# Optimization experiments

Measured on AMD Instinct MI355X. Metric: run time of the kernel, lower is better.

Reference implementation:

```python
import jax, jax.numpy as jnp
import numpy as np

F_DIM = 128; K_RBF = 64; NBLOCKS = 3; NUM_SCC = 1; IBEGIN = 4
N_RES_INT = 2; N_RES_AT = 2; N_RES_OUT = 1
NUM_OUTPUTS = 2001; NOUTS = NUM_OUTPUTS + 4  # +4 charge-equilibration channels when num_scc>0
N_ATOMS = 10000; DEG = 32; N_EDGES = N_ATOMS * DEG; NMOL = 64
CUTOFF = 10.0
LOG2 = 0.6931471805599453


def ssp(x):
    # shifted softplus
    return jax.nn.softplus(x) - LOG2


def _residual(x, W1, b1, W2, b2):
    y = ssp(x) @ W1 + b1
    return x + ssp(y) @ W2 + b2


def _forward(R, M, QaAlpha, QaBeta,
             em_W0, em_b0, em_W1, em_b1, em_W2, em_b2,
             iWrbf, iWi, ibi, iWj, ibj, irW1, irb1, irW2, irb2, iWout, ibout, iu,
             arW1, arb1, arW2, arb2, orW1, orb1, orW2, orb2, oW,
             Z, idx_i, idx_j, mol_idx):
    N = R.shape[0]
    dt = R.dtype
    # --- interatomic distances via neighbor gather ---
    Dvec = R[idx_i] - R[idx_j]                                # [E,3]
    Dij = jnp.sqrt(jax.nn.relu(jnp.sum(Dvec * Dvec, -1)))     # [E]
    # --- PhysNet-style exp-Gaussian RBF expansion with smooth cutoff ---
    mu = jnp.linspace(np.exp(-CUTOFF), 1.0, K_RBF).astype(dt)
    gamma = jnp.asarray((K_RBF / (2.0 * (1.0 - np.exp(-CUTOFF)))) ** 2, dt)
    t = Dij / CUTOFF
    cut = jnp.where(Dij < CUTOFF, 1.0 - 6.0 * t**5 + 15.0 * t**4 - 10.0 * t**3, 0.0)
    rbf = cut[:, None] * jnp.exp(-gamma * (jnp.exp(-Dij)[:, None] - mu) ** 2)  # [E,K]

    seg_mol = lambda v: jax.ops.segment_sum(v, mol_idx, num_segments=NMOL)
    Zf = Z.astype(dt)[:, None]
    QaA, QaB = QaAlpha, QaBeta
    QAlpha_mol = seg_mol(QaA)
    QBeta_mol = seg_mol(QaB)
    outputs = None
    nhloss = jnp.asarray(0.0, dt)
    for j in range(NUM_SCC + 1):
        # elemental-modes embedding: f = [Z, M, QaAlpha, QaBeta] -> F
        f = jnp.concatenate([Zf, M[:, None], QaA[:, None], QaB[:, None]], 1)  # [N,4]
        h = ssp(f @ em_W0 + em_b0)
        h = ssp(h @ em_W1 + em_b1)
        x = h @ em_W2 + em_b2                                 # [N,F]
        outputs = jnp.zeros((N, NOUTS), dt)
        nhloss = jnp.asarray(0.0, dt)
        lastout2 = None
        for i in range(NBLOCKS):
            # --- interaction (message passing: gather -> multiply -> segment_sum) ---
            xa = ssp(x)
            g = rbf @ iWrbf[i]                                # [E,F]
            xi = ssp(xa @ iWi[i] + ibi[i])                    # [N,F]
            xj = ssp(xa @ iWj[i] + ibj[i])                    # [N,F]
            m = xi + jax.ops.segment_sum(g * xj[idx_j], idx_i, num_segments=N)
            for r in range(N_RES_INT):
                m = _residual(m, irW1[i, r], irb1[i, r], irW2[i, r], irb2[i, r])
            m = ssp(m)
            x = iu[i] * x + m @ iWout[i] + ibout[i]           # gated update
            for r in range(N_RES_AT):
                x = _residual(x, arW1[i, r], arb1[i, r], arW2[i, r], arb2[i, r])
            # --- output block ---
            xo = x
            for r in range(N_RES_OUT):
                xo = _residual(xo, orW1[i, r], orb1[i, r], orW2[i, r], orb2[i, r])
            out = ssp(xo) @ oW[i]                             # [N,NOUTS]
            outputs = outputs + out
            if j == NUM_SCC:
                out2 = out[IBEGIN:] ** 2                      # row slice, as in source
                if i > 0:
                    nhloss = nhloss + jnp.mean(out2 / (out2 + lastout2 + 1e-7))
                lastout2 = out2
        # --- NSE charge equilibration (per-molecule segment sums) ---
        QaA_n, faA = outputs[:, 0], outputs[:, 1]
        QaB_n, faB = outputs[:, 2], outputs[:, 3]
        QaA = QaA_n + faA * ((QAlpha_mol - seg_mol(QaA_n)) / seg_mol(faA))[mol_idx]
        QaB = QaB_n + faB * ((QBeta_mol - seg_mol(QaB_n)) / seg_mol(faB))[mol_idx]
    outputs = outputs[:, IBEGIN:]
    outputs = jnp.concatenate([outputs[:, :1], jax.nn.relu(outputs[:, 1:])], 1)
    return outputs, Dij, nhloss


def setup_inputs() -> dict:
    key = jax.random.key(0)
    ks = iter(jax.random.split(key, 64))
    nrm = lambda shp, scale: jax.random.normal(next(ks), shp, jnp.float32) * scale
    F, K, B = F_DIM, K_RBF, NBLOCKS
    s = F ** -0.5
    inp = {}
    inp["R"] = jax.random.uniform(next(ks), (N_ATOMS, 3), jnp.float32, 0.0, 12.0)
    inp["M"] = jax.random.uniform(next(ks), (N_ATOMS,), jnp.float32, 1.0, 32.0)
    inp["QaAlpha"] = nrm((N_ATOMS,), 0.1)
    inp["QaBeta"] = nrm((N_ATOMS,), 0.1)
    # elemental-modes MLP 4 -> F -> F -> F
    inp["em_W0"] = nrm((4, F), 0.5); inp["em_b0"] = nrm((F,), 0.01)
    inp["em_W1"] = nrm((F, F), s);   inp["em_b1"] = nrm((F,), 0.01)
    inp["em_W2"] = nrm((F, F), s);   inp["em_b2"] = nrm((F,), 0.01)
    # interaction blocks (stacked over NBLOCKS)
    inp["iWrbf"] = nrm((B, K, F), K ** -0.5)
    inp["iWi"] = nrm((B, F, F), s); inp["ibi"] = nrm((B, F), 0.01)
    inp["iWj"] = nrm((B, F, F), s); inp["ibj"] = nrm((B, F), 0.01)
    inp["irW1"] = nrm((B, N_RES_INT, F, F), s); inp["irb1"] = nrm((B, N_RES_INT, F), 0.01)
    inp["irW2"] = nrm((B, N_RES_INT, F, F), s); inp["irb2"] = nrm((B, N_RES_INT, F), 0.01)
    inp["iWout"] = nrm((B, F, F), s); inp["ibout"] = nrm((B, F), 0.01)
    inp["iu"] = jnp.ones((B, F), jnp.float32)
    inp["arW1"] = nrm((B, N_RES_AT, F, F), s); inp["arb1"] = nrm((B, N_RES_AT, F), 0.01)
    inp["arW2"] = nrm((B, N_RES_AT, F, F), s); inp["arb2"] = nrm((B, N_RES_AT, F), 0.01)
    inp["orW1"] = nrm((B, N_RES_OUT, F, F), s); inp["orb1"] = nrm((B, N_RES_OUT, F), 0.01)
    inp["orW2"] = nrm((B, N_RES_OUT, F, F), s); inp["orb2"] = nrm((B, N_RES_OUT, F), 0.01)
    inp["oW"] = nrm((B, F, NOUTS), s)
    # integer graph structure
    inp["Z"] = jax.random.randint(next(ks), (N_ATOMS,), 1, 36, jnp.int32)
    idx_i = jnp.repeat(jnp.arange(N_ATOMS, dtype=jnp.int32), DEG)
    rnd = jax.random.randint(next(ks), (N_EDGES,), 1, N_ATOMS, jnp.int32)
    inp["idx_i"] = idx_i
    inp["idx_j"] = (idx_i + rnd) % N_ATOMS  # never self -> Dij > 0
    inp["mol_idx"] = ((jnp.arange(N_ATOMS) * NMOL) // N_ATOMS).astype(jnp.int32)
    return inp


def reference(R, M, QaAlpha, QaBeta,
              em_W0, em_b0, em_W1, em_b1, em_W2, em_b2,
              iWrbf, iWi, ibi, iWj, ibj, irW1, irb1, irW2, irb2, iWout, ibout, iu,
              arW1, arb1, arW2, arb2, orW1, orb1, orW2, orb2, oW,
              Z, idx_i, idx_j, mol_idx):
    return _forward(R, M, QaAlpha, QaBeta,
                    em_W0, em_b0, em_W1, em_b1, em_W2, em_b2,
                    iWrbf, iWi, ibi, iWj, ibj, irW1, irb1, irW2, irb2, iWout, ibout, iu,
                    arW1, arb1, arW2, arb2, orW1, orb1, orW2, orb2, oW,
                    Z, idx_i, idx_j, mol_idx)
```

## Files before the change

kernel.cpp:

```cpp
#include <hip/hip_runtime.h>
#include <math.h>

#define NA 10000
#define FD 128
#define KR 64
#define DEGC 32
#define NE (NA*DEGC)
#define NOUTS_C 2005
#define NOUT_FINAL 2001

typedef __attribute__((ext_vector_type(8))) short bh8;
typedef __attribute__((ext_vector_type(4))) float fx4;

__device__ __forceinline__ float sspf(float x){
    float ex = __expf(-fabsf(x));
    return fmaxf(x, 0.0f) + __logf(1.0f + ex) - 0.6931471805599453f;
}
__device__ __forceinline__ unsigned short f2bf(float x){
    unsigned int u = __float_as_uint(x);
    unsigned int r = (u + 0x7fffu + ((u >> 16) & 1u)) >> 16;
    return (unsigned short)r;
}
__device__ __forceinline__ float bf2f(unsigned short u){
    return __uint_as_float(((unsigned int)u) << 16);
}
__device__ __forceinline__ fx4 mfma16(bh8 a, bh8 b, fx4 c){
    return __builtin_amdgcn_mfma_f32_16x16x32_bf16(a, b, c, 0, 0, 0);
}
__device__ __forceinline__ void gll16(const void* g, void* l){
    __builtin_amdgcn_global_load_lds(
        (const __attribute__((address_space(1))) unsigned int*)g,
        (__attribute__((address_space(3))) unsigned int*)l, 16, 0, 0);
}

__global__ void k_dij(const float* __restrict__ R, const int* __restrict__ idx_i,
                      const int* __restrict__ idx_j, float* __restrict__ dij_out){
    int e = blockIdx.x*256 + threadIdx.x;
    if (e >= NE) return;
    int i = idx_i[e], j = idx_j[e];
    float dx = R[i*3+0] - R[j*3+0];
    float dy = R[i*3+1] - R[j*3+1];
    float dz = R[i*3+2] - R[j*3+2];
    dij_out[e] = sqrtf(fmaxf(dx*dx + dy*dy + dz*dz, 0.0f));
}

__global__ void k_init(const float* __restrict__ QaAin, const float* __restrict__ QaBin,
                       const int* __restrict__ mol, float* __restrict__ QaA,
                       float* __restrict__ QaB, float* __restrict__ QAmol,
                       float* __restrict__ QBmol){
    int a = blockIdx.x*256 + threadIdx.x;
    if (a >= NA) return;
    float qa = QaAin[a], qb = QaBin[a];
    QaA[a] = qa; QaB[a] = qb;
    int m = mol[a];
    atomicAdd(&QAmol[m], qa);
    atomicAdd(&QBmol[m], qb);
}

__global__ void k_cvtW(const float* __restrict__ em_W1, const float* __restrict__ em_W2,
                       const float* __restrict__ iWi, const float* __restrict__ iWj,
                       const float* __restrict__ iWout, const float* __restrict__ irW1,
                       const float* __restrict__ irW2, const float* __restrict__ arW1,
                       const float* __restrict__ arW2, const float* __restrict__ orW1,
                       const float* __restrict__ orW2, short* __restrict__ img){
    int gid = blockIdx.x*256 + threadIdx.x;
    if (gid >= 41*2048) return;
    int m = gid >> 11;
    int f = gid & 2047;
    int l15 = f & 15, t = f >> 4;
    int g = t & 3, u = t >> 2;
    int kk = u & 3, cg = u >> 2;
    const float* src; int mm;
    if      (m < 1){ src = em_W1; mm = m; }
    else if (m < 2){ src = em_W2; mm = m-1; }
    else if (m < 5){ src = iWi;   mm = m-2; }
    else if (m < 8){ src = iWj;   mm = m-5; }
    else if (m < 11){ src = iWout; mm = m-8; }
    else if (m < 17){ src = irW1;  mm = m-11; }
    else if (m < 23){ src = irW2;  mm = m-17; }
    else if (m < 29){ src = arW1;  mm = m-23; }
    else if (m < 35){ src = arW2;  mm = m-29; }
    else if (m < 38){ src = orW1;  mm = m-35; }
    else            { src = orW2;  mm = m-38; }
    src += (size_t)mm * 16384;
    int n = cg*16 + l15;
    int k0 = (kk*4 + g)*8;
    bh8 pk;
    #pragma unroll
    for (int j = 0; j < 8; ++j) pk[j] = (short)f2bf(src[(k0+j)*128 + n]);
    *(bh8*)&img[m*16384 + f*8] = pk;
}

__global__ void k_cvtB(const float* __restrict__ em_b1, const float* __restrict__ em_b2,
                       const float* __restrict__ ibi, const float* __restrict__ ibj,
                       const float* __restrict__ ibout, const float* __restrict__ irb1,
                       const float* __restrict__ irb2, const float* __restrict__ arb1,
                       const float* __restrict__ arb2, const float* __restrict__ orb1,
                       const float* __restrict__ orb2, const float* __restrict__ iu,
                       float* __restrict__ bimg){
    int gid = blockIdx.x*256 + threadIdx.x;
    if (gid >= 44*128) return;
    int m = gid >> 7, c = gid & 127;
    float v;
    if      (m < 1)  v = em_b1[c];
    else if (m < 2)  v = em_b2[c];
    else if (m < 5)  v = ibi[(m-2)*128+c];
    else if (m < 8)  v = ibj[(m-5)*128+c];
    else if (m < 11) v = ibout[(m-8)*128+c];
    else if (m < 17) v = irb1[(m-11)*128+c];
    else if (m < 23) v = irb2[(m-17)*128+c];
    else if (m < 29) v = arb1[(m-23)*128+c];
    else if (m < 35) v = arb2[(m-29)*128+c];
    else if (m < 38) v = orb1[(m-35)*128+c];
    else if (m < 41) v = orb2[(m-38)*128+c];
    else             v = iu[(m-41)*128+c];
    bimg[gid] = v;
}

__global__ void k_cvt_wrbf(const float* __restrict__ iWrbf, short* __restrict__ img){
    int gid = blockIdx.x*256 + threadIdx.x;
    if (gid >= 3*1024) return;
    int i = gid >> 10;
    int loc = gid & 1023;
    int n = loc >> 3, s = loc & 7;
    const float* src = iWrbf + (size_t)i*8192;
    int kbase = (s ^ (n&7)) * 8;
    bh8 pk;
    #pragma unroll
    for (int j = 0; j < 8; ++j) pk[j] = (short)f2bf(src[(kbase+j)*128 + n]);
    *(bh8*)&img[i*8192 + n*64 + s*8] = pk;
}

__global__ void k_cvt_oW(const float* __restrict__ oW, short* __restrict__ img){
    int gid = blockIdx.x*256 + threadIdx.x;
    if (gid >= 98304) return;
    int l15 = gid & 15;
    int g = (gid >> 4) & 3;
    int nt = (gid >> 6) & 7;
    int rest = gid >> 9;
    int kk2 = rest % 12, cg = rest / 12;
    int seg = kk2 >> 2;
    int n = cg*128 + nt*16 + l15;
    int kbase = (kk2 & 3)*32 + g*8;
    bh8 pk;
    #pragma unroll
    for (int j = 0; j < 8; ++j){
        float v = (n < NOUTS_C) ? oW[((size_t)seg*128 + kbase + j)*NOUTS_C + n] : 0.0f;
        pk[j] = (short)f2bf(v);
    }
    *(bh8*)&img[(size_t)gid*8] = pk;
}

__device__ __forceinline__ void loadB8(const short* __restrict__ W, int g, int l15, int wv, bh8 b[8]){
    const bh8* Wf = (const bh8*)W;
    const int cgA = wv*2, cgB = wv*2 + 1;
    #pragma unroll
    for (int kk = 0; kk < 4; ++kk){
        b[kk]   = Wf[((cgA*4+kk)*4+g)*16 + l15];
        b[4+kk] = Wf[((cgB*4+kk)*4+g)*16 + l15];
    }
}
__device__ __forceinline__ void gemmB(const short* As, const bh8 b[8], int g, int l15, fx4 acc[2]){
    #pragma unroll
    for (int kk = 0; kk < 4; ++kk){
        int q = kk*4 + g;
        bh8 a = *(const bh8*)&As[l15*128 + ((q ^ (l15&7))*8)];
        acc[0] = mfma16(a, b[kk],   acc[0]);
        acc[1] = mfma16(a, b[4+kk], acc[1]);
    }
}
#define ZACC2 { acc[0]=(fx4){0,0,0,0}; acc[1]=(fx4){0,0,0,0}; }

__device__ __forceinline__ void epiS_ts(short* dst, fx4 acc[2], const float* b,
                                        int g, int c0, int c1){
    float b0 = b[c0], b1 = b[c1];
    #pragma unroll
    for (int r = 0; r < 4; ++r){
        int row = g*4 + r;
        dst[row*128 + (((c0>>3) ^ (row&7))*8) + (c0&7)] = (short)f2bf(sspf(acc[0][r] + b0));
        dst[row*128 + (((c1>>3) ^ (row&7))*8) + (c1&7)] = (short)f2bf(sspf(acc[1][r] + b1));
    }
}
__device__ __forceinline__ void epiS_xadd(float xr[2][4], fx4 acc[2], const float* b,
                                          int c0, int c1){
    float b0 = b[c0], b1 = b[c1];
    #pragma unroll
    for (int r = 0; r < 4; ++r){
        xr[0][r] += acc[0][r] + b0;
        xr[1][r] += acc[1][r] + b1;
    }
}
__device__ __forceinline__ void writeS_xr(short* dst, float xr[2][4], int g, int c0, int c1){
    #pragma unroll
    for (int r = 0; r < 4; ++r){
        int row = g*4 + r;
        dst[row*128 + (((c0>>3) ^ (row&7))*8) + (c0&7)] = (short)f2bf(sspf(xr[0][r]));
        dst[row*128 + (((c1>>3) ^ (row&7))*8) + (c1&7)] = (short)f2bf(sspf(xr[1][r]));
    }
}
__device__ __forceinline__ void storeS_xr(float* dst, float xr[2][4], int r0, int g, int c0, int c1){
    #pragma unroll
    for (int r = 0; r < 4; ++r){
        int row = r0 + g*4 + r;
        dst[(size_t)row*FD + c0] = xr[0][r];
        dst[(size_t)row*FD + c1] = xr[1][r];
    }
}
__device__ __forceinline__ void storeS_ssp(float* dst, fx4 acc[2], const float* b,
                                           int r0, int g, int c0, int c1){
    float b0 = b[c0], b1 = b[c1];
    #pragma unroll
    for (int r = 0; r < 4; ++r){
        int row = r0 + g*4 + r;
        dst[(size_t)row*FD + c0] = sspf(acc[0][r] + b0);
        dst[(size_t)row*FD + c1] = sspf(acc[1][r] + b1);
    }
}
__device__ __forceinline__ void stage_A16(short* As, const float* src, int r0, int tid){
    int row = tid >> 4, cb = tid & 15;
    const float* p = src + (size_t)(r0+row)*FD + cb*8;
    float4 u = *(const float4*)p, v = *(const float4*)(p+4);
    float vv[8] = {u.x,u.y,u.z,u.w,v.x,v.y,v.z,v.w};
    bh8 pk;
    #pragma unroll
    for (int t = 0; t < 8; ++t) pk[t] = (short)f2bf(sspf(vv[t]));
    *(bh8*)&As[row*128 + ((cb ^ (row&7))*8)] = pk;
}

__global__ __launch_bounds__(256) void k_pre(
    const short* __restrict__ wimg, const float* __restrict__ bimg,
    const int* __restrict__ Z, const float* __restrict__ M,
    const float* __restrict__ QaA, const float* __restrict__ QaB,
    const float* __restrict__ em_W0, const float* __restrict__ em_b0,
    float* __restrict__ x, float* __restrict__ xi, float* __restrict__ xj)
{
    __shared__ __align__(16) short As[2048];
    __shared__ __align__(16) short Ts[2048];
    __shared__ float fs[16][4];
    const int tid = threadIdx.x, wv = tid>>6, ln = tid&63, g = ln>>4, l15 = ln&15;
    const int r0 = blockIdx.x*16;
    const int c0 = wv*32 + l15, c1 = c0 + 16;
    bh8 bU[8], bV[8];
    if (tid < 64){
        int rr = tid>>2, k = tid&3;
        int a = r0 + rr;
        fs[rr][k] = (k==0) ? (float)Z[a] : (k==1) ? M[a] : (k==2) ? QaA[a] : QaB[a];
    }
    __syncthreads();
    {
        int row = tid>>4, cb = tid&15;
        bh8 pk;
        #pragma unroll
        for (int t = 0; t < 8; ++t){
            int c = cb*8 + t;
            float v = sspf(em_b0[c] + fs[row][0]*em_W0[c] + fs[row][1]*em_W0[128+c]
                           + fs[row][2]*em_W0[256+c] + fs[row][3]*em_W0[384+c]);
            pk[t] = (short)f2bf(v);
        }
        *(bh8*)&As[row*128 + ((cb ^ (row&7))*8)] = pk;
    }
    loadB8(wimg + 0*16384, g, l15, wv, bU);
    __syncthreads();
    fx4 acc[2];
    float xr[2][4];
    ZACC2; gemmB(As, bU, g, l15, acc);
    loadB8(wimg + 1*16384, g, l15, wv, bV);
    epiS_ts(Ts, acc, bimg + 0*128, g, c0, c1);
    __syncthreads();
    ZACC2; gemmB(Ts, bV, g, l15, acc);
    loadB8(wimg + 2*16384, g, l15, wv, bU);
    {
        const float* b = bimg + 1*128;
        float b0 = b[c0], b1 = b[c1];
        #pragma unroll
        for (int r = 0; r < 4; ++r){
            xr[0][r] = acc[0][r] + b0;
            xr[1][r] = acc[1][r] + b1;
        }
    }
    storeS_xr(x, xr, r0, g, c0, c1);
    writeS_xr(As, xr, g, c0, c1);
    __syncthreads();
    ZACC2; gemmB(As, bU, g, l15, acc);
    loadB8(wimg + 5*16384, g, l15, wv, bV);
    storeS_ssp(xi, acc, bimg + 2*128, r0, g, c0, c1);
    ZACC2; gemmB(As, bV, g, l15, acc);
    storeS_ssp(xj, acc, bimg + 5*128, r0, g, c0, c1);
}

__global__ __launch_bounds__(256) void k_post(
    const short* __restrict__ wimg, const float* __restrict__ bimg,
    const float* __restrict__ mb, float* __restrict__ x,
    short* __restrict__ Aimg, float* __restrict__ xi, float* __restrict__ xj,
    int i, int dodual)
{
    __shared__ __align__(16) short As[2048];
    __shared__ __align__(16) short Ts[2048];
    const int tid = threadIdx.x, wv = tid>>6, ln = tid&63, g = ln>>4, l15 = ln&15;
    const int r0 = blockIdx.x*16;
    const int c0 = wv*32 + l15, c1 = c0 + 16;
    bh8 bU[8], bV[8];
    float xr[2][4];
    #pragma unroll
    for (int r = 0; r < 4; ++r){
        size_t row = (size_t)(r0 + g*4 + r);
        xr[0][r] = mb[row*FD + c0];
        xr[1][r] = mb[row*FD + c1];
    }
    stage_A16(As, mb, r0, tid);
    loadB8(wimg + (size_t)(11+2*i)*16384, g, l15, wv, bU);
    __syncthreads();
    fx4 acc[2];
    ZACC2; gemmB(As, bU, g, l15, acc);
    loadB8(wimg + (size_t)(17+2*i)*16384, g, l15, wv, bV);
    epiS_ts(Ts, acc, bimg + (11+2*i)*128, g, c0, c1);
    __syncthreads();
    ZACC2; gemmB(Ts, bV, g, l15, acc);
    loadB8(wimg + (size_t)(12+2*i)*16384, g, l15, wv, bU);
    epiS_xadd(xr, acc, bimg + (17+2*i)*128, c0, c1);
    writeS_xr(As, xr, g, c0, c1);
    __syncthreads();
    ZACC2; gemmB(As, bU, g, l15, acc);
    loadB8(wimg + (size_t)(18+2*i)*16384, g, l15, wv, bV);
    epiS_ts(Ts, acc, bimg + (12+2*i)*128, g, c0, c1);
    __syncthreads();
    ZACC2; gemmB(Ts, bV, g, l15, acc);
    loadB8(wimg + (size_t)(8+i)*16384, g, l15, wv, bU);
    epiS_xadd(xr, acc, bimg + (18+2*i)*128, c0, c1);
    writeS_xr(As, xr, g, c0, c1);
    __syncthreads();
    ZACC2; gemmB(As, bU, g, l15, acc);
    loadB8(wimg + (size_t)(23+2*i)*16384, g, l15, wv, bV);
    {
        const float* bb = bimg + (8+i)*128;
        const float* uu = bimg + (41+i)*128;
        float b0 = bb[c0], b1 = bb[c1], u0 = uu[c0], u1 = uu[c1];
        #pragma unroll
        for (int r = 0; r < 4; ++r){
            size_t row = (size_t)(r0 + g*4 + r);
            xr[0][r] = u0*x[row*FD + c0] + acc[0][r] + b0;
            xr[1][r] = u1*x[row*FD + c1] + acc[1][r] + b1;
        }
    }
    writeS_xr(Ts, xr, g, c0, c1);
    __syncthreads();
    ZACC2; gemmB(Ts, bV, g, l15, acc);
    loadB8(wimg + (size_t)(29+2*i)*16384, g, l15, wv, bU);
    epiS_ts(As, acc, bimg + (23+2*i)*128, g, c0, c1);
    __syncthreads();
    ZACC2; gemmB(As, bU, g, l15, acc);
    loadB8(wimg + (size_t)(24+2*i)*16384, g, l15, wv, bV);
    epiS_xadd(xr, acc, bimg + (29+2*i)*128, c0, c1);
    writeS_xr(Ts, xr, g, c0, c1);
    __syncthreads();
    ZACC2; gemmB(Ts, bV, g, l15, acc);
    loadB8(wimg + (size_t)(30+2*i)*16384, g, l15, wv, bU);
    epiS_ts(As, acc, bimg + (24+2*i)*128, g, c0, c1);
    __syncthreads();
    ZACC2; gemmB(As, bU, g, l15, acc);
    loadB8(wimg + (size_t)(dodual ? (3+i) : (35+i))*16384, g, l15, wv, bV);
    epiS_xadd(xr, acc, bimg + (30+2*i)*128, c0, c1);
    storeS_xr(x, xr, r0, g, c0, c1);
    writeS_xr(Ts, xr, g, c0, c1);
    __syncthreads();
    if (dodual){
        ZACC2; gemmB(Ts, bV, g, l15, acc);
        loadB8(wimg + (size_t)(6+i)*16384, g, l15, wv, bU);
        storeS_ssp(xi, acc, bimg + (3+i)*128, r0, g, c0, c1);
        ZACC2; gemmB(Ts, bU, g, l15, acc);
        loadB8(wimg + (size_t)(35+i)*16384, g, l15, wv, bV);
        storeS_ssp(xj, acc, bimg + (6+i)*128, r0, g, c0, c1);
        ZACC2; gemmB(Ts, bV, g, l15, acc);
        loadB8(wimg + (size_t)(38+i)*16384, g, l15, wv, bU);
        epiS_ts(As, acc, bimg + (35+i)*128, g, c0, c1);
    } else {
        ZACC2; gemmB(Ts, bV, g, l15, acc);
        loadB8(wimg + (size_t)(38+i)*16384, g, l15, wv, bU);
        epiS_ts(As, acc, bimg + (35+i)*128, g, c0, c1);
    }
    __syncthreads();
    ZACC2; gemmB(As, bU, g, l15, acc);
    {
        const float* bb = bimg + (38+i)*128;
        float b0 = bb[c0], b1 = bb[c1];
        #pragma unroll
        for (int r = 0; r < 4; ++r){
            int row = r0 + g*4 + r;
            float v0 = xr[0][r] + acc[0][r] + b0;
            float v1 = xr[1][r] + acc[1][r] + b1;
            int k0 = i*128 + c0, k1 = i*128 + c1;
            Aimg[(size_t)row*384 + (((k0>>3) ^ (row&7))*8) + (k0&7)] = (short)f2bf(sspf(v0));
            Aimg[(size_t)row*384 + (((k1>>3) ^ (row&7))*8) + (k1&7)] = (short)f2bf(sspf(v1));
        }
    }
}

__global__ __launch_bounds__(256) void k_agg_mfma(
    const float* __restrict__ dij, const short* __restrict__ wri,
    const int* __restrict__ idxj, const float* __restrict__ xi,
    const float* __restrict__ xj, float* __restrict__ mout,
    float gamma, float mu0, float dmu)
{
    __shared__ short Rb[256*64];
    __shared__ short Wr[128*64];
    __shared__ int Jd[256];
    const int tid = threadIdx.x;
    const int wv = tid >> 6, ln = tid & 63;
    const int e0 = blockIdx.x * 256;
    {
        const char* g2 = (const char*)wri;
        char* l2 = (char*)Wr;
        #pragma unroll
        for (int i = 0; i < 4; ++i){
            int off = wv*4096 + i*1024;
            gll16(g2 + off + ln*16, l2 + off);
        }
        Jd[tid] = idxj[e0 + tid];
    }
    {
        float d = dij[e0 + tid];
        float t = d * 0.1f;
        float cut = 0.0f;
        if (d < 10.0f){
            float t2 = t*t, t3 = t2*t, t4 = t2*t2, t5 = t4*t;
            cut = 1.0f - 6.0f*t5 + 15.0f*t4 - 10.0f*t3;
        }
        float ed = __expf(-d);
        int row = tid;
        #pragma unroll
        for (int s = 0; s < 8; ++s){
            bh8 pk;
            #pragma unroll
            for (int jj = 0; jj < 8; ++jj){
                float u = ed - (mu0 + (float)(s*8+jj)*dmu);
                pk[jj] = (short)f2bf(cut * __expf(-gamma*u*u));
            }
            *(bh8*)&Rb[row*64 + ((s ^ (row&7))*8)] = pk;
        }
    }
    __syncthreads();
    const int g = ln >> 4, l15 = ln & 15;
    bh8 a[4][2];
    #pragma unroll
    for (int mt = 0; mt < 4; ++mt){
        int el = wv*64 + mt*16 + l15;
        #pragma unroll
        for (int kk = 0; kk < 2; ++kk)
            a[mt][kk] = *(const bh8*)&Rb[el*64 + (((kk*4+g) ^ (el&7))*8)];
    }
    float pa[2][8];
    #pragma unroll
    for (int q = 0; q < 8; ++q){ pa[0][q]=0.f; pa[1][q]=0.f; }
    #pragma unroll
    for (int h = 0; h < 2; ++h){
        fx4 acc[4][4];
        #pragma unroll
        for (int mt = 0; mt < 4; ++mt)
            #pragma unroll
            for (int nt = 0; nt < 4; ++nt) acc[mt][nt] = (fx4){0,0,0,0};
        #pragma unroll
        for (int kk = 0; kk < 2; ++kk){
            #pragma unroll
            for (int nt = 0; nt < 4; ++nt){
                int n = h*64 + nt*16 + l15;
                bh8 b = *(const bh8*)&Wr[n*64 + (((kk*4+g) ^ (n&7))*8)];
                #pragma unroll
                for (int mt = 0; mt < 4; ++mt)
                    acc[mt][nt] = mfma16(a[mt][kk], b, acc[mt][nt]);
            }
        }
        #pragma unroll
        for (int mt = 0; mt < 4; ++mt){
            int at = mt >> 1;
            int jv[4];
            #pragma unroll
            for (int r = 0; r < 4; ++r) jv[r] = Jd[wv*64 + mt*16 + g*4 + r];
            #pragma unroll
            for (int nt = 0; nt < 4; ++nt){
                int col = h*64 + nt*16 + l15;
                float s = 0.f;
                #pragma unroll
                for (int r = 0; r < 4; ++r)
                    s += acc[mt][nt][r] * xj[(size_t)jv[r]*FD + col];
                pa[at][h*4+nt] += s;
            }
        }
    }
    #pragma unroll
    for (int at = 0; at < 2; ++at)
        #pragma unroll
        for (int q = 0; q < 8; ++q){
            float v = pa[at][q];
            v += __shfl_xor(v, 16);
            v += __shfl_xor(v, 32);
            pa[at][q] = v;
        }
    if (g == 0){
        #pragma unroll
        for (int at = 0; at < 2; ++at){
            int ga = blockIdx.x*8 + wv*2 + at;
            #pragma unroll
            for (int q = 0; q < 8; ++q){
                int col = (q>>2)*64 + (q&3)*16 + l15;
                mout[(size_t)ga*FD + col] = xi[(size_t)ga*FD + col] + pa[at][q];
            }
        }
    }
}

__global__ void k_out4all(const short* __restrict__ Aimg, const float* __restrict__ oW,
                          float* __restrict__ out4){
    int gid = blockIdx.x*256 + threadIdx.x;
    int a = gid >> 6;
    int lane = threadIdx.x & 63;
    if (a >= NA) return;
    float p0=0.f, p1=0.f, p2=0.f, p3=0.f;
    #pragma unroll
    for (int seg = 0; seg < 3; ++seg){
        const float* oWs = oW + (size_t)seg*FD*NOUTS_C;
        int k0 = seg*128 + lane, k1 = k0 + 64;
        float y0 = bf2f((unsigned short)Aimg[(size_t)a*384 + (((k0>>3) ^ (a&7))*8) + (k0&7)]);
        float y1 = bf2f((unsigned short)Aimg[(size_t)a*384 + (((k1>>3) ^ (a&7))*8) + (k1&7)]);
        const float* w0 = oWs + (size_t)lane*NOUTS_C;
        const float* w1 = oWs + (size_t)(lane+64)*NOUTS_C;
        p0 += y0*w0[0] + y1*w1[0];
        p1 += y0*w0[1] + y1*w1[1];
        p2 += y0*w0[2] + y1*w1[2];
        p3 += y0*w0[3] + y1*w1[3];
    }
    #pragma unroll
    for (int off = 32; off > 0; off >>= 1){
        p0 += __shfl_down(p0, off);
        p1 += __shfl_down(p1, off);
        p2 += __shfl_down(p2, off);
        p3 += __shfl_down(p3, off);
    }
    if (lane == 0){
        out4[a*4+0] = p0; out4[a*4+1] = p1;
        out4[a*4+2] = p2; out4[a*4+3] = p3;
    }
}

__global__ void k_molsum(const float* __restrict__ out4, const int* __restrict__ mol,
                         float* __restrict__ sums){
    int a = blockIdx.x*256 + threadIdx.x;
    if (a >= NA) return;
    int m = mol[a];
    atomicAdd(&sums[m],     out4[a*4+0]);
    atomicAdd(&sums[64+m],  out4[a*4+1]);
    atomicAdd(&sums[128+m], out4[a*4+2]);
    atomicAdd(&sums[192+m], out4[a*4+3]);
}

__global__ void k_qaupd(const float* __restrict__ out4, const int* __restrict__ mol,
                        const float* __restrict__ sums, const float* __restrict__ QAmol,
                        const float* __restrict__ QBmol, float* __restrict__ QaA,
                        float* __restrict__ QaB){
    int a = blockIdx.x*256 + threadIdx.x;
    if (a >= NA) return;
    int m = mol[a];
    float qa_n = out4[a*4+0], fa = out4[a*4+1];
    float qb_n = out4[a*4+2], fb = out4[a*4+3];
    QaA[a] = qa_n + fa * ((QAmol[m] - sums[m])     / sums[64+m]);
    QaB[a] = qb_n + fb * ((QBmol[m] - sums[128+m]) / sums[192+m]);
}

__global__ __launch_bounds__(256) void k_final3(
    const short* __restrict__ Aimg, const short* __restrict__ oWfrag,
    float* __restrict__ outp, float* __restrict__ nh_acc)
{
    __shared__ __align__(16) short As[64*384];
    const int tid = threadIdx.x, wv = tid>>6, ln = tid&63, g = ln>>4, l15 = ln&15;
    const int a0 = blockIdx.x * 64;
    const int cg = blockIdx.y;
    {
        const char* gA = (const char*)(Aimg + (size_t)a0*384);
        char* lA = (char*)As;
        #pragma unroll
        for (int i = 0; i < 12; ++i){
            int off = wv*12288 + i*1024;
            gll16(gA + off + ln*16, lA + off);
        }
    }
    __syncthreads();
    const bh8* Bf = (const bh8*)oWfrag + (size_t)cg*12*8*64;
    const int arow = wv*16 + l15;
    fx4 osum[8], p2[8];
    #pragma unroll
    for (int nt = 0; nt < 8; ++nt){ osum[nt] = (fx4){0,0,0,0}; p2[nt] = (fx4){0,0,0,0}; }
    float nh = 0.f;
    for (int seg = 0; seg < 3; ++seg){
        fx4 acc[8];
        #pragma unroll
        for (int nt = 0; nt < 8; ++nt) acc[nt] = (fx4){0,0,0,0};
        #pragma unroll
        for (int kkl = 0; kkl < 4; ++kkl){
            int kk2 = seg*4 + kkl;
            bh8 b[8];
            #pragma unroll
            for (int nt = 0; nt < 8; ++nt)
                b[nt] = Bf[((size_t)kk2*8 + nt)*64 + g*16 + l15];
            int s = kk2*4 + g;
            bh8 a = *(const bh8*)&As[arow*384 + ((s ^ (arow&7))*8)];
            #pragma unroll
            for (int nt = 0; nt < 8; ++nt)
                acc[nt] = mfma16(a, b[nt], acc[nt]);
        }
        #pragma unroll
        for (int nt = 0; nt < 8; ++nt)
        #pragma unroll
        for (int r = 0; r < 4; ++r){
            float o = acc[nt][r];
            osum[nt][r] += o;
            if (seg > 0){
                int A = a0 + wv*16 + g*4 + r;
                int col = cg*128 + nt*16 + l15;
                if (A >= 4 && A < NA && col < NOUTS_C){
                    float o2 = o*o;
                    float den = o2 + p2[nt][r] + 1e-7f;
                    float rr;
                    asm("v_rcp_f32 %0, %1" : "=v"(rr) : "v"(den));
                    nh += o2 * rr;
                }
            }
            p2[nt][r] = o*o;
        }
    }
    #pragma unroll
    for (int nt = 0; nt < 8; ++nt){
        int col = cg*128 + nt*16 + l15;
        #pragma unroll
        for (int r = 0; r < 4; ++r){
            int A = a0 + wv*16 + g*4 + r;
            if (A < NA && col >= 4 && col < NOUTS_C){
                float v = osum[nt][r];
                if (col > 4) v = fmaxf(v, 0.f);
                outp[(size_t)A*NOUT_FINAL + (col - 4)] = v;
            }
        }
    }
    #pragma unroll
    for (int off = 32; off > 0; off >>= 1) nh += __shfl_down(nh, off);
    if (ln == 0) atomicAdd(nh_acc, nh);
}

__global__ void k_finalize(const float* __restrict__ nh_acc, float* __restrict__ nh_out){
    *nh_out = *nh_acc * (1.0f / (float)((NA - 4) * NOUTS_C));
}

extern "C" void kernel_launch(void* const* d_in, const int* in_sizes, int n_in,
                              void* d_out, int out_size, void* d_ws, size_t ws_size,
                              hipStream_t stream)
{
    const float* R       = (const float*)d_in[0];
    const float* M       = (const float*)d_in[1];
    const float* QaAlpha = (const float*)d_in[2];
    const float* QaBeta  = (const float*)d_in[3];
    const float* em_W0   = (const float*)d_in[4];
    const float* em_b0   = (const float*)d_in[5];
    const float* em_W1   = (const float*)d_in[6];
    const float* em_b1   = (const float*)d_in[7];
    const float* em_W2   = (const float*)d_in[8];
    const float* em_b2   = (const float*)d_in[9];
    const float* iWrbf   = (const float*)d_in[10];
    const float* iWi     = (const float*)d_in[11];
    const float* ibi     = (const float*)d_in[12];
    const float* iWj     = (const float*)d_in[13];
    const float* ibj     = (const float*)d_in[14];
    const float* irW1    = (const float*)d_in[15];
    const float* irb1    = (const float*)d_in[16];
    const float* irW2    = (const float*)d_in[17];
    const float* irb2    = (const float*)d_in[18];
    const float* iWout   = (const float*)d_in[19];
    const float* ibout   = (const float*)d_in[20];
    const float* iu      = (const float*)d_in[21];
    const float* arW1    = (const float*)d_in[22];
    const float* arb1    = (const float*)d_in[23];
    const float* arW2    = (const float*)d_in[24];
    const float* arb2    = (const float*)d_in[25];
    const float* orW1    = (const float*)d_in[26];
    const float* orb1    = (const float*)d_in[27];
    const float* orW2    = (const float*)d_in[28];
    const float* orb2    = (const float*)d_in[29];
    const float* oW      = (const float*)d_in[30];
    const int*   Z       = (const int*)d_in[31];
    const int*   idx_i   = (const int*)d_in[32];
    const int*   idx_j   = (const int*)d_in[33];
    const int*   mol     = (const int*)d_in[34];

    float* out    = (float*)d_out;
    float* dij    = out + (size_t)NA*NOUT_FINAL;
    float* nh_out = dij + NE;

    float* fbase = (float*)d_ws;
    size_t fo = 0;
    float* x    = fbase + fo; fo += (size_t)NA*FD;
    float* xi   = fbase + fo; fo += (size_t)NA*FD;
    float* xj   = fbase + fo; fo += (size_t)NA*FD;
    float* mb   = fbase + fo; fo += (size_t)NA*FD;
    float* out4 = fbase + fo; fo += (size_t)NA*4;
    float* sums = fbase + fo; fo += 256;
    float* QAmol= fbase + fo; fo += 64;
    float* QBmol= fbase + fo; fo += 64;
    float* nhac = fbase + fo; fo += 1;
    float* QaA  = fbase + fo; fo += NA;
    float* QaB  = fbase + fo; fo += NA;
    float* bimg = fbase + fo; fo += 44*128;
    size_t sboff = ((fo*4 + 63) / 64) * 64;
    short* sbase = (short*)((char*)d_ws + sboff);
    size_t so = 0;
    short* wimg   = sbase + so; so += (size_t)41*16384;
    short* wrbf   = sbase + so; so += (size_t)3*8192;
    short* oWfrag = sbase + so; so += (size_t)98304*8;
    short* Aimg   = sbase + so; so += (size_t)10048*384;

    hipMemsetAsync(sums, 0, (size_t)(256 + 64 + 64 + 1)*sizeof(float), stream);
    hipMemsetAsync(Aimg + (size_t)10000*384, 0, (size_t)48*384*sizeof(short), stream);

    k_cvtW<<<(41*2048+255)/256, 256, 0, stream>>>(em_W1, em_W2, iWi, iWj, iWout,
                                                  irW1, irW2, arW1, arW2, orW1, orW2, wimg);
    k_cvtB<<<(44*128+255)/256, 256, 0, stream>>>(em_b1, em_b2, ibi, ibj, ibout,
                                                 irb1, irb2, arb1, arb2, orb1, orb2, iu, bimg);
    k_cvt_wrbf<<<(3*1024+255)/256, 256, 0, stream>>>(iWrbf, wrbf);
    k_cvt_oW<<<(98304+255)/256, 256, 0, stream>>>(oW, oWfrag);

    k_dij<<<(NE+255)/256, 256, 0, stream>>>(R, idx_i, idx_j, dij);
    k_init<<<(NA+255)/256, 256, 0, stream>>>(QaAlpha, QaBeta, mol, QaA, QaB, QAmol, QBmol);

    double expn = exp(-10.0);
    float gamma = (float)pow(64.0/(2.0*(1.0-expn)), 2.0);
    float mu0 = (float)expn;
    float dmu = (float)((1.0-expn)/63.0);

    for (int j = 0; j <= 1; ++j){
        k_pre<<<625, 256, 0, stream>>>(wimg, bimg, Z, M, QaA, QaB, em_W0, em_b0, x, xi, xj);
        for (int i = 0; i < 3; ++i){
            k_agg_mfma<<<1250, 256, 0, stream>>>(dij, wrbf + (size_t)i*8192, idx_j, xi, xj, mb,
                                                 gamma, mu0, dmu);
            k_post<<<625, 256, 0, stream>>>(wimg, bimg, mb, x, Aimg, xi, xj, i, (i<2) ? 1 : 0);
        }
        if (j == 0){
            k_out4all<<<(NA*64)/256, 256, 0, stream>>>(Aimg, oW, out4);
            k_molsum<<<(NA+255)/256, 256, 0, stream>>>(out4, mol, sums);
            k_qaupd<<<(NA+255)/256, 256, 0, stream>>>(out4, mol, sums, QAmol, QBmol, QaA, QaB);
        }
    }
    k_final3<<<dim3(157,16), 256, 0, stream>>>(Aimg, oWfrag, out, nhac);
    k_finalize<<<1, 1, 0, stream>>>(nhac, nh_out);
}
```

Measured before the change: 963.6 us.

## Restructure final output GEMM to stage results in LDS for coalesced stores

The final output kernel now handles 32 atoms per block and loops over 8 column groups inside each block, with 4 waves split into 2 row tiles by 2 column halves. Each column group's results are written to a shared-memory tile and then stored to the 2001-wide output rows with contiguous lane-wise writes. The old version scattered strided stores directly from MFMA fragments. The aim is better write coalescing on the large output and reuse of the staged A tile across column groups, at the cost of extra barriers and a smaller, less parallel grid.

Result: slower. 993.0 us (+3.1%).

```diff
diff --git a/kernel.cpp b/kernel.cpp
--- a/kernel.cpp
+++ b/kernel.cpp
@@ -2,6 +2,7 @@
 #include <math.h>
 
 #define NA 10000
+#define NAP 10048
 #define FD 128
 #define KR 64
 #define DEGC 32
@@ -565,77 +566,94 @@
     QaB[a] = qb_n + fb * ((QBmol[m] - sums[128+m]) / sums[192+m]);
 }
 
-__global__ __launch_bounds__(256) void k_final3(
+__global__ __launch_bounds__(256) void k_final5(
     const short* __restrict__ Aimg, const short* __restrict__ oWfrag,
     float* __restrict__ outp, float* __restrict__ nh_acc)
 {
-    __shared__ __align__(16) short As[64*384];
+    __shared__ __align__(16) short As[32*384];
+    __shared__ float Cs[32][132];
     const int tid = threadIdx.x, wv = tid>>6, ln = tid&63, g = ln>>4, l15 = ln&15;
-    const int a0 = blockIdx.x * 64;
-    const int cg = blockIdx.y;
+    const int a0 = blockIdx.x * 32;
+    const int rt = wv & 1, nth = wv >> 1;
     {
         const char* gA = (const char*)(Aimg + (size_t)a0*384);
         char* lA = (char*)As;
         #pragma unroll
-        for (int i = 0; i < 12; ++i){
-            int off = wv*12288 + i*1024;
-            gll16(gA + off + ln*16, lA + off);
-        }
-    }
-    __syncthreads();
-    const bh8* Bf = (const bh8*)oWfrag + (size_t)cg*12*8*64;
-    const int arow = wv*16 + l15;
-    fx4 osum[8], p2[8];
-    #pragma unroll
-    for (int nt = 0; nt < 8; ++nt){ osum[nt] = (fx4){0,0,0,0}; p2[nt] = (fx4){0,0,0,0}; }
+        for (int t = 0; t < 6; ++t)
+            gll16(gA + t*4096 + tid*16, lA + t*4096 + tid*16);
+    }
+    __syncthreads();
+    const int arow = rt*16 + l15;
     float nh = 0.f;
-    for (int seg = 0; seg < 3; ++seg){
-        fx4 acc[8];
-        #pragma unroll
-        for (int nt = 0; nt < 8; ++nt) acc[nt] = (fx4){0,0,0,0};
-        #pragma unroll
-        for (int kkl = 0; kkl < 4; ++kkl){
-            int kk2 = seg*4 + kkl;
-            bh8 b[8];
-            #pragma unroll
-            for (int nt = 0; nt < 8; ++nt)
-                b[nt] = Bf[((size_t)kk2*8 + nt)*64 + g*16 + l15];
-            int s = kk2*4 + g;
-            bh8 a = *(const bh8*)&As[arow*384 + ((s ^ (arow&7))*8)];
-            #pragma unroll
-            for (int nt = 0; nt < 8; ++nt)
-                acc[nt] = mfma16(a, b[nt], acc[nt]);
-        }
-        #pragma unroll
-        for (int nt = 0; nt < 8; ++nt)
-        #pragma unroll
-        for (int r = 0; r < 4; ++r){
-            float o = acc[nt][r];
-            osum[nt][r] += o;
-            if (seg > 0){
-                int A = a0 + wv*16 + g*4 + r;
-                int col = cg*128 + nt*16 + l15;
-                if (A >= 4 && A < NA && col < NOUTS_C){
-                    float o2 = o*o;
-                    float den = o2 + p2[nt][r] + 1e-7f;
-                    float rr;
-                    asm("v_rcp_f32 %0, %1" : "=v"(rr) : "v"(den));
-                    nh += o2 * rr;
+    for (int cgl = 0; cgl < 8; ++cgl){
+        int cg = blockIdx.y*8 + cgl;
+        const bh8* Bf = (const bh8*)oWfrag + (size_t)cg*6144;
+        fx4 osum[4], p2[4];
+        #pragma unroll
+        for (int ntl = 0; ntl < 4; ++ntl){ osum[ntl] = (fx4){0,0,0,0}; p2[ntl] = (fx4){0,0,0,0}; }
+        #pragma unroll
+        for (int seg = 0; seg < 3; ++seg){
+            fx4 acc[4];
+            #pragma unroll
+            for (int ntl = 0; ntl < 4; ++ntl) acc[ntl] = (fx4){0,0,0,0};
+            #pragma unroll
+            for (int kkl = 0; kkl < 4; ++kkl){
+                int kk2 = seg*4 + kkl;
+                int s = kk2*4 + g;
+                bh8 a = *(const bh8*)&As[arow*384 + ((s ^ (arow&7))*8)];
+                #pragma unroll
+                for (int ntl = 0; ntl < 4; ++ntl){
+                    int nt = nth*4 + ntl;
+                    bh8 b = Bf[((kk2*8 + nt)*4 + g)*16 + l15];
+                    acc[ntl] = mfma16(a, b, acc[ntl]);
                 }
             }
-            p2[nt][r] = o*o;
-        }
-    }
-    #pragma unroll
-    for (int nt = 0; nt < 8; ++nt){
-        int col = cg*128 + nt*16 + l15;
-        #pragma unroll
-        for (int r = 0; r < 4; ++r){
-            int A = a0 + wv*16 + g*4 + r;
-            if (A < NA && col >= 4 && col < NOUTS_C){
-                float v = osum[nt][r];
-                if (col > 4) v = fmaxf(v, 0.f);
-                outp[(size_t)A*NOUT_FINAL + (col - 4)] = v;
+            #pragma unroll
+            for (int ntl = 0; ntl < 4; ++ntl)
+            #pragma unroll
+            for (int r = 0; r < 4; ++r){
+                float o = acc[ntl][r];
+                osum[ntl][r] += o;
+                if (seg > 0){
+                    int A = a0 + rt*16 + g*4 + r;
+                    int col = cg*128 + (nth*4+ntl)*16 + l15;
+                    if (A >= 4 && A < NA && col < NOUTS_C){
+                        float o2 = o*o;
+                        float den = o2 + p2[ntl][r] + 1e-7f;
+                        float rr;
+                        asm("v_rcp_f32 %0, %1" : "=v"(rr) : "v"(den));
+                        nh += o2 * rr;
+                    }
+                }
+                p2[ntl][r] = o*o;
+            }
+        }
+        __syncthreads();
+        #pragma unroll
+        for (int ntl = 0; ntl < 4; ++ntl){
+            int c = (nth*4+ntl)*16 + l15;
+            #pragma unroll
+            for (int r = 0; r < 4; ++r)
+                Cs[rt*16 + g*4 + r][c] = osum[ntl][r];
+        }
+        __syncthreads();
+        const int cgbase = cg*128;
+        #pragma unroll
+        for (int r8 = 0; r8 < 8; ++r8){
+            int row = wv*8 + r8;
+            int A = a0 + row;
+            if (A < NA){
+                size_t orow = (size_t)A*NOUT_FINAL;
+                #pragma unroll
+                for (int e = 0; e < 2; ++e){
+                    int c = e*64 + ln;
+                    int colg = cgbase + c;
+                    if (colg >= 4 && colg < NOUTS_C){
+                        float v = Cs[row][c];
+                        if (colg > 4) v = fmaxf(v, 0.f);
+                        outp[orow + (colg - 4)] = v;
+                    }
+                }
             }
         }
     }
@@ -712,10 +730,10 @@
     short* wimg   = sbase + so; so += (size_t)41*16384;
     short* wrbf   = sbase + so; so += (size_t)3*8192;
     short* oWfrag = sbase + so; so += (size_t)98304*8;
-    short* Aimg   = sbase + so; so += (size_t)10048*384;
+    short* Aimg   = sbase + so; so += (size_t)NAP*384;
 
     hipMemsetAsync(sums, 0, (size_t)(256 + 64 + 64 + 1)*sizeof(float), stream);
-    hipMemsetAsync(Aimg + (size_t)10000*384, 0, (size_t)48*384*sizeof(short), stream);
+    hipMemsetAsync(Aimg + (size_t)NA*384, 0, (size_t)(NAP-NA)*384*sizeof(short), stream);
 
     k_cvtW<<<(41*2048+255)/256, 256, 0, stream>>>(em_W1, em_W2, iWi, iWj, iWout,
                                                   irW1, irW2, arW1, arW2, orW1, orW2, wimg);
@@ -745,6 +763,6 @@
             k_qaupd<<<(NA+255)/256, 256, 0, stream>>>(out4, mol, sums, QAmol, QBmol, QaA, QaB);
         }
     }
-    k_final3<<<dim3(157,16), 256, 0, stream>>>(Aimg, oWfrag, out, nhac);
+    k_final5<<<dim3(314,2), 256, 0, stream>>>(Aimg, oWfrag, out, nhac);
     k_finalize<<<1, 1, 0, stream>>>(nhac, nh_out);
 }
```

## Read A fragments directly from global and stage output through LDS for coalesced stores

Applied to the files above, without the earlier changes.

The final output GEMM no longer stages the 64x384 activation tile into shared memory. Each wave now loads its A fragments straight from global memory, and B fragments are loaded one per MFMA instead of batched. The accumulated results are written to a padded LDS buffer and then stored row by row with lanes covering contiguous columns, so the writes to the large output matrix are coalesced. This trades a block-wide LDS load and barrier for per-wave global A reads, aiming to reduce the cost of the scattered output stores.

Result: slower. 991.6 us (+2.9%).

```diff
diff --git a/kernel.cpp b/kernel.cpp
--- a/kernel.cpp
+++ b/kernel.cpp
@@ -2,6 +2,7 @@
 #include <math.h>
 
 #define NA 10000
+#define NAP 10048
 #define FD 128
 #define KR 64
 #define DEGC 32
@@ -565,30 +566,20 @@
     QaB[a] = qb_n + fb * ((QBmol[m] - sums[128+m]) / sums[192+m]);
 }
 
-__global__ __launch_bounds__(256) void k_final3(
+__global__ __launch_bounds__(256) void k_final6(
     const short* __restrict__ Aimg, const short* __restrict__ oWfrag,
     float* __restrict__ outp, float* __restrict__ nh_acc)
 {
-    __shared__ __align__(16) short As[64*384];
+    __shared__ float Cs[4][16][132];
     const int tid = threadIdx.x, wv = tid>>6, ln = tid&63, g = ln>>4, l15 = ln&15;
-    const int a0 = blockIdx.x * 64;
+    const int r0 = blockIdx.x*64 + wv*16;
     const int cg = blockIdx.y;
-    {
-        const char* gA = (const char*)(Aimg + (size_t)a0*384);
-        char* lA = (char*)As;
-        #pragma unroll
-        for (int i = 0; i < 12; ++i){
-            int off = wv*12288 + i*1024;
-            gll16(gA + off + ln*16, lA + off);
-        }
-    }
-    __syncthreads();
-    const bh8* Bf = (const bh8*)oWfrag + (size_t)cg*12*8*64;
-    const int arow = wv*16 + l15;
+    const bh8* Bf = (const bh8*)oWfrag + (size_t)cg*6144;
     fx4 osum[8], p2[8];
     #pragma unroll
-    for (int nt = 0; nt < 8; ++nt){ osum[nt] = (fx4){0,0,0,0}; p2[nt] = (fx4){0,0,0,0}; }
+    for (int nt = 0; nt < 8; ++nt){ osum[nt]=(fx4){0,0,0,0}; p2[nt]=(fx4){0,0,0,0}; }
     float nh = 0.f;
+    #pragma unroll
     for (int seg = 0; seg < 3; ++seg){
         fx4 acc[8];
         #pragma unroll
@@ -596,15 +587,13 @@
         #pragma unroll
         for (int kkl = 0; kkl < 4; ++kkl){
             int kk2 = seg*4 + kkl;
-            bh8 b[8];
+            int s = kk2*4 + g;
+            bh8 a = *(const bh8*)&Aimg[(size_t)(r0+l15)*384 + ((s ^ (l15&7))*8)];
             #pragma unroll
-            for (int nt = 0; nt < 8; ++nt)
-                b[nt] = Bf[((size_t)kk2*8 + nt)*64 + g*16 + l15];
-            int s = kk2*4 + g;
-            bh8 a = *(const bh8*)&As[arow*384 + ((s ^ (arow&7))*8)];
-            #pragma unroll
-            for (int nt = 0; nt < 8; ++nt)
-                acc[nt] = mfma16(a, b[nt], acc[nt]);
+            for (int nt = 0; nt < 8; ++nt){
+                bh8 b = Bf[((kk2*8 + nt)*4 + g)*16 + l15];
+                acc[nt] = mfma16(a, b, acc[nt]);
+            }
         }
         #pragma unroll
         for (int nt = 0; nt < 8; ++nt)
@@ -613,7 +602,7 @@
             float o = acc[nt][r];
             osum[nt][r] += o;
             if (seg > 0){
-                int A = a0 + wv*16 + g*4 + r;
+                int A = r0 + g*4 + r;
                 int col = cg*128 + nt*16 + l15;
                 if (A >= 4 && A < NA && col < NOUTS_C){
                     float o2 = o*o;
@@ -627,15 +616,24 @@
         }
     }
     #pragma unroll
-    for (int nt = 0; nt < 8; ++nt){
-        int col = cg*128 + nt*16 + l15;
-        #pragma unroll
-        for (int r = 0; r < 4; ++r){
-            int A = a0 + wv*16 + g*4 + r;
-            if (A < NA && col >= 4 && col < NOUTS_C){
-                float v = osum[nt][r];
-                if (col > 4) v = fmaxf(v, 0.f);
-                outp[(size_t)A*NOUT_FINAL + (col - 4)] = v;
+    for (int nt = 0; nt < 8; ++nt)
+        #pragma unroll
+        for (int r = 0; r < 4; ++r)
+            Cs[wv][g*4 + r][nt*16 + l15] = osum[nt][r];
+    const int cgbase = cg*128;
+    #pragma unroll
+    for (int r8 = 0; r8 < 16; ++r8){
+        int A = r0 + r8;
+        if (A < NA){
+            size_t orow = (size_t)A*NOUT_FINAL;
+            #pragma unroll
+            for (int e = 0; e < 2; ++e){
+                int colg = cgbase + e*64 + ln;
+                if (colg >= 4 && colg < NOUTS_C){
+                    float v = Cs[wv][r8][e*64 + ln];
+                    if (colg > 4) v = fmaxf(v, 0.f);
+                    outp[orow + (colg - 4)] = v;
+                }
             }
         }
     }
@@ -712,10 +710,10 @@
     short* wimg   = sbase + so; so += (size_t)41*16384;
     short* wrbf   = sbase + so; so += (size_t)3*8192;
     short* oWfrag = sbase + so; so += (size_t)98304*8;
-    short* Aimg   = sbase + so; so += (size_t)10048*384;
+    short* Aimg   = sbase + so; so += (size_t)NAP*384;
 
     hipMemsetAsync(sums, 0, (size_t)(256 + 64 + 64 + 1)*sizeof(float), stream);
-    hipMemsetAsync(Aimg + (size_t)10000*384, 0, (size_t)48*384*sizeof(short), stream);
+    hipMemsetAsync(Aimg + (size_t)NA*384, 0, (size_t)(NAP-NA)*384*sizeof(short), stream);
 
     k_cvtW<<<(41*2048+255)/256, 256, 0, stream>>>(em_W1, em_W2, iWi, iWj, iWout,
                                                   irW1, irW2, arW1, arW2, orW1, orW2, wimg);
@@ -745,6 +743,6 @@
             k_qaupd<<<(NA+255)/256, 256, 0, stream>>>(out4, mol, sums, QAmol, QBmol, QaA, QaB);
         }
     }
-    k_final3<<<dim3(157,16), 256, 0, stream>>>(Aimg, oWfrag, out, nhac);
+    k_final6<<<dim3(157,16), 256, 0, stream>>>(Aimg, oWfrag, out, nhac);
     k_finalize<<<1, 1, 0, stream>>>(nhac, nh_out);
 }
```
